# Kernel tuning notes

Measured on AMD Instinct MI355X. Metric: run time of the kernel, lower is better.

Reference implementation:

```python
import jax, jax.numpy as jnp
import numpy as np

IN_FEATURES = 512
OUT_FEATURES = 512
GRID_SIZE = 5
SPLINE_ORDER = 3
GRID_RANGE = (-3.0, 3.0)


def make_grid():
    h = (GRID_RANGE[1] - GRID_RANGE[0]) / GRID_SIZE
    g = jnp.arange(-SPLINE_ORDER, GRID_SIZE + SPLINE_ORDER + 1, dtype=jnp.float32) * h + GRID_RANGE[0]
    return jnp.broadcast_to(g, (IN_FEATURES, g.shape[0]))  # [in, grid_size+2*order+1]


def b_splines(x, grid):
    # x: [N, in] -> bases: [N, in, grid_size + spline_order]
    x = x[..., None]  # [N, in, 1]
    bases = ((x >= grid[:, :-1]) & (x < grid[:, 1:])).astype(x.dtype)
    for k in range(1, SPLINE_ORDER + 1):
        left = (x - grid[:, :-(k + 1)]) / (grid[:, k:-1] - grid[:, :-(k + 1)])
        right = (grid[:, k + 1:] - x) / (grid[:, k + 1:] - grid[:, 1:-k])
        bases = left * bases[..., :-1] + right * bases[..., 1:]
    return bases


def setup_inputs() -> dict:
    key = jax.random.key(0)
    k1, k2, k3, k4 = jax.random.split(key, 4)
    N = 32768
    bound = 1.0 / np.sqrt(IN_FEATURES)  # kaiming_uniform-ish scale
    x = jax.random.normal(k1, (N, IN_FEATURES), dtype=jnp.float32)
    base_weight = jax.random.uniform(k2, (OUT_FEATURES, IN_FEATURES), minval=-bound, maxval=bound, dtype=jnp.float32)
    spline_weight = jax.random.normal(k3, (OUT_FEATURES, IN_FEATURES, GRID_SIZE + SPLINE_ORDER), dtype=jnp.float32) * 0.1
    spline_scaler = jax.random.uniform(k4, (OUT_FEATURES, IN_FEATURES), minval=-bound, maxval=bound, dtype=jnp.float32)
    grid = make_grid()
    return {"x": x, "base_weight": base_weight, "spline_weight": spline_weight, "spline_scaler": spline_scaler, "grid": grid}


def reference(x, base_weight, spline_weight, spline_scaler, grid):
    # base branch: SiLU(x) @ W_base^T
    base_out = jnp.einsum('ni,oi->no', jax.nn.silu(x), base_weight)
    # spline branch: Cox-de Boor basis then GEMM with scaled spline weights
    b = b_splines(x, grid)  # [N, in, G+K]
    sw = spline_weight * spline_scaler[..., None]  # [out, in, G+K]
    spline_out = jnp.einsum('nik,oik->no', b, sw)
    return base_out + spline_out
```

## Files before the change

### kernel.cpp

```cpp
#include <hip/hip_runtime.h>

#define NSAMP 32768
#define INF 512
#define OUTF 512
#define NB 8
#define KSP 4096
#define KTOT 4608

typedef __attribute__((ext_vector_type(8))) short bf16x8;
typedef __attribute__((ext_vector_type(4))) float f32x4;

typedef __attribute__((address_space(1))) void gas_void;
typedef __attribute__((address_space(3))) void las_void;
#define GLL16(g, l) __builtin_amdgcn_global_load_lds( \
    (const gas_void*)(g), (las_void*)(l), 16, 0, 0)

__device__ __forceinline__ unsigned short f2bf(float f) {
  unsigned int u = __float_as_uint(f);
  u += 0x7fffu + ((u >> 16) & 1u);
  return (unsigned short)(u >> 16);
}

__device__ __forceinline__ unsigned pack_rn(float lo, float hi) {
  return __builtin_amdgcn_perm(__float_as_uint(hi) + 0x8000u,
                               __float_as_uint(lo) + 0x8000u, 0x07060302u);
}

__device__ __forceinline__ uint4 kan_basis_vec(float xv) {
  float t = __builtin_fmaf(xv, 1.0f / 1.2f, 5.5f);
  float cf = floorf(t);
  float u = t - cf;
  int j0 = (int)cf - 3;
  float omu = 1.0f - u;
  float u2 = u * u, u3 = u2 * u;
  float omu2 = omu * omu;
  float w0 = omu2 * omu;
  float w1 = __builtin_fmaf(3.f, u3, __builtin_fmaf(-6.f, u2, 4.f));
  float w2 = __builtin_fmaf(-3.f, u3,
              __builtin_fmaf(3.f, u2, __builtin_fmaf(3.f, u, 1.f)));
  float w3 = u3;
  unsigned P0 = pack_rn(w0, w1);
  unsigned P1 = pack_rn(w2, w3);
  int p = j0 & 1;
  unsigned Q0 = p ? (P0 << 16) : P0;
  unsigned Q1 = p ? __builtin_amdgcn_alignbit(P1, P0, 16) : P1;
  unsigned Q2 = p ? (P1 >> 16) : 0u;
  int D = j0 >> 1;
  uint4 r;
  r.x = (D == 0) ? Q0 : (D == -1) ? Q1 : (D == -2) ? Q2 : 0u;
  r.y = (D == 1) ? Q0 : (D ==  0) ? Q1 : (D == -1) ? Q2 : 0u;
  r.z = (D == 2) ? Q0 : (D ==  1) ? Q1 : (D ==  0) ? Q2 : 0u;
  r.w = (D == 3) ? Q0 : (D ==  2) ? Q1 : (D ==  1) ? Q2 : 0u;
  return r;
}

__global__ __launch_bounds__(256) void kan_prep_w(
    const float* __restrict__ bw, const float* __restrict__ sw,
    const float* __restrict__ sc, unsigned short* __restrict__ W) {
  int idx = blockIdx.x * 256 + threadIdx.x;
  float scv = sc[idx] * (1.0f / 6.0f);
  float4 s0 = ((const float4*)sw)[idx * 2 + 0];
  float4 s1 = ((const float4*)sw)[idx * 2 + 1];
  unsigned short v[8];
  v[0] = f2bf(s0.x * scv); v[1] = f2bf(s0.y * scv);
  v[2] = f2bf(s0.z * scv); v[3] = f2bf(s0.w * scv);
  v[4] = f2bf(s1.x * scv); v[5] = f2bf(s1.y * scv);
  v[6] = f2bf(s1.z * scv); v[7] = f2bf(s1.w * scv);
  int o = idx >> 9, i = idx & 511;
  *(bf16x8*)(W + (size_t)o * KTOT + i * NB) = *(bf16x8*)v;
  W[(size_t)o * KTOT + KSP + i] = f2bf(bw[idx]);
}

__device__ __forceinline__ void mfma_chunk(
    const unsigned short* As, const unsigned short* Bs,
    f32x4 acc[4][8], int wm, int wn, int frow, int quad) {
  const int fr7 = frow & 7;
  #pragma unroll
  for (int ks = 0; ks < 2; ++ks) {
    bf16x8 av[4], bv[8];
    const int sa = ((ks * 4 + quad) ^ fr7) * 8;
    #pragma unroll
    for (int f = 0; f < 4; ++f)
      av[f] = *(const bf16x8*)&As[(wm + f * 16 + frow) * 64 + sa];
    #pragma unroll
    for (int g = 0; g < 8; ++g)
      bv[g] = *(const bf16x8*)&Bs[(wn + g * 16 + frow) * 64 + sa];
    #pragma unroll
    for (int mf = 0; mf < 4; ++mf)
      #pragma unroll
      for (int nf = 0; nf < 8; ++nf)
        acc[mf][nf] = __builtin_amdgcn_mfma_f32_16x16x32_bf16(
            av[mf], bv[nf], acc[mf][nf], 0, 0, 0);
  }
}

__global__ __launch_bounds__(256, 2) void kan_fused(
    const float* __restrict__ x, const unsigned short* __restrict__ W,
    float* __restrict__ out) {
  __shared__ __align__(16) unsigned short As[128 * 64];
  __shared__ __align__(16) unsigned short Bs[256 * 64];
  const int tid = threadIdx.x;
  const int wave = tid >> 6;
  const int lane = tid & 63;
  const int frow = lane & 15;
  const int quad = lane >> 4;
  const int lr = lane >> 3;
  const int lc = lane & 7;
  const int mtile = blockIdx.x & 255;
  const int ntile = blockIdx.x >> 8;
  const int wm = (wave & 1) << 6;
  const int wn = (wave >> 1) << 7;

  f32x4 acc[4][8];
  #pragma unroll
  for (int i = 0; i < 4; ++i)
    #pragma unroll
    for (int j = 0; j < 8; ++j)
      acc[i][j] = (f32x4){0.f, 0.f, 0.f, 0.f};

  const unsigned short* bgp[8];
  #pragma unroll
  for (int is = 0; is < 8; ++is)
    bgp[is] = W + (size_t)(ntile * 256 + wave * 64 + is * 8 + lr) * KTOT +
              ((lc ^ lr) * 8);
  const float* xb = x + (size_t)mtile * 128 * INF;
  const float* xp[4];
  #pragma unroll
  for (int is = 0; is < 4; ++is)
    xp[is] = xb + (size_t)(wave * 32 + is * 8 + lr) * INF + lc;

  float xc[4];
  #pragma unroll
  for (int is = 0; is < 4; ++is) xc[is] = xp[is][0];

  for (int kc = 0; kc < 64; ++kc) {
    #pragma unroll
    for (int is = 0; is < 8; ++is) {
      GLL16(bgp[is], &Bs[(wave * 64 + is * 8) * 64]);
      bgp[is] += 64;
    }
    float xn[4];
    const int knext = ((kc + 1) & 63) * 8;
    #pragma unroll
    for (int is = 0; is < 4; ++is) xn[is] = xp[is][knext];

    #pragma unroll
    for (int is = 0; is < 4; ++is) {
      const int row = wave * 32 + is * 8 + lr;
      uint4 bb = kan_basis_vec(xc[is]);
      *(uint4*)&As[row * 64 + ((lc ^ lr) * 8)] = bb;
    }
    __syncthreads();
    mfma_chunk(As, Bs, acc, wm, wn, frow, quad);
    __syncthreads();
    #pragma unroll
    for (int is = 0; is < 4; ++is) xc[is] = xn[is];
  }

  for (int sc = 0; sc < 8; ++sc) {
    float4 v0[4], v1[4];
    #pragma unroll
    for (int is = 0; is < 4; ++is) {
      const int row = wave * 32 + is * 8 + lr;
      const float* xr = xb + (size_t)row * INF + sc * 64 + lc * 8;
      v0[is] = *(const float4*)xr;
      v1[is] = *(const float4*)(xr + 4);
    }
    #pragma unroll
    for (int is = 0; is < 8; ++is) {
      GLL16(bgp[is], &Bs[(wave * 64 + is * 8) * 64]);
      bgp[is] += 64;
    }
    #pragma unroll
    for (int is = 0; is < 4; ++is) {
      const int row = wave * 32 + is * 8 + lr;
      float vv[8] = {v0[is].x, v0[is].y, v0[is].z, v0[is].w,
                     v1[is].x, v1[is].y, v1[is].z, v1[is].w};
      float s[8];
      #pragma unroll
      for (int e = 0; e < 8; ++e)
        s[e] = vv[e] * __builtin_amdgcn_rcpf(1.0f + __expf(-vv[e]));
      uint4 pk;
      pk.x = pack_rn(s[0], s[1]);
      pk.y = pack_rn(s[2], s[3]);
      pk.z = pack_rn(s[4], s[5]);
      pk.w = pack_rn(s[6], s[7]);
      *(uint4*)&As[row * 64 + ((lc ^ lr) * 8)] = pk;
    }
    __syncthreads();
    mfma_chunk(As, Bs, acc, wm, wn, frow, quad);
    __syncthreads();
  }

  const size_t m0 = (size_t)mtile * 128;
  const int n0 = ntile * 256;
  #pragma unroll
  for (int mf = 0; mf < 4; ++mf)
    #pragma unroll
    for (int nf = 0; nf < 8; ++nf)
      #pragma unroll
      for (int r = 0; r < 4; ++r)
        out[(m0 + wm + mf * 16 + quad * 4 + r) * OUTF + (n0 + wn + nf * 16 + frow)] =
            acc[mf][nf][r];
}

__global__ __launch_bounds__(256) void kan_naive(
    const float* __restrict__ x, const float* __restrict__ bw,
    const float* __restrict__ sw, const float* __restrict__ sc,
    float* __restrict__ out) {
  int idx = blockIdx.x * 256 + threadIdx.x;
  int n = idx >> 9, o = idx & 511;
  const float* xr = x + (size_t)n * INF;
  float acc = 0.f;
  for (int i = 0; i < INF; ++i) {
    float xv = xr[i];
    float sil = xv / (1.0f + __expf(-xv));
    float t = (xv + 6.6f) * (1.0f / 1.2f);
    float cf = floorf(t);
    float u = t - cf;
    int j0 = (int)cf - 3;
    float omu = 1.0f - u;
    float u2 = u * u, u3 = u2 * u;
    float w[4];
    w[0] = (1.0f / 6.0f) * omu * omu * omu;
    w[1] = (1.0f / 6.0f) * (3.0f * u3 - 6.0f * u2 + 4.0f);
    w[2] = (1.0f / 6.0f) * (-3.0f * u3 + 3.0f * u2 + 3.0f * u + 1.0f);
    w[3] = (1.0f / 6.0f) * u3;
    int wi = o * INF + i;
    acc += sil * bw[wi];
    float sp = 0.f;
    #pragma unroll
    for (int m = 0; m < 4; ++m) {
      int j = j0 + m;
      if ((unsigned)j < 8u) sp += w[m] * sw[wi * NB + j];
    }
    acc += sp * sc[wi];
  }
  out[idx] = acc;
}

extern "C" void kernel_launch(void* const* d_in, const int* in_sizes, int n_in,
                              void* d_out, int out_size, void* d_ws, size_t ws_size,
                              hipStream_t stream) {
  const float* x  = (const float*)d_in[0];
  const float* bw = (const float*)d_in[1];
  const float* sw = (const float*)d_in[2];
  const float* sc = (const float*)d_in[3];
  float* out = (float*)d_out;

  const size_t wbytes = (size_t)OUTF * KTOT * 2;
  if (ws_size >= wbytes) {
    unsigned short* W = (unsigned short*)d_ws;
    kan_prep_w<<<(OUTF * INF) / 256, 256, 0, stream>>>(bw, sw, sc, W);
    kan_fused<<<(NSAMP / 128) * (OUTF / 256), 256, 0, stream>>>(x, W, out);
  } else {
    kan_naive<<<(NSAMP * OUTF) / 256, 256, 0, stream>>>(x, bw, sw, sc, out);
  }
}
```

Measured before the change: 250.1 us.

## Double-buffer spline weight tiles in LDS and overlap prefetch with MFMA

Splits the B-tile LDS buffer into two halves so the next spline-weight chunk is fetched with global_load_lds while MFMAs run on the current one. The basis tile for the following chunk is now written after the compute barrier instead of before it. A hand-placed s_waitcnt vmcnt(12) plus raw s_barrier replaces __syncthreads, and setprio raises wave priority around the MFMA blocks. This raises LDS use to about 80KB per block, and the fixed vmcnt count is fragile: on the last spline iteration it may not wait for every load of the final weight buffer.

```diff
diff --git a/kernel.cpp b/kernel.cpp
--- a/kernel.cpp
+++ b/kernel.cpp
@@ -98,7 +98,7 @@
     const float* __restrict__ x, const unsigned short* __restrict__ W,
     float* __restrict__ out) {
   __shared__ __align__(16) unsigned short As[128 * 64];
-  __shared__ __align__(16) unsigned short Bs[256 * 64];
+  __shared__ __align__(16) unsigned short Bs[2][256 * 64];
   const int tid = threadIdx.x;
   const int wave = tid >> 6;
   const int lane = tid & 63;
@@ -129,32 +129,48 @@
   for (int is = 0; is < 4; ++is)
     xp[is] = xb + (size_t)(wave * 32 + is * 8 + lr) * INF + lc;
 
-  float xc[4];
-  #pragma unroll
-  for (int is = 0; is < 4; ++is) xc[is] = xp[is][0];
+  {
+    #pragma unroll
+    for (int is = 0; is < 4; ++is) {
+      const int row = wave * 32 + is * 8 + lr;
+      uint4 bb = kan_basis_vec(xp[is][0]);
+      *(uint4*)&As[row * 64 + ((lc ^ lr) * 8)] = bb;
+    }
+    #pragma unroll
+    for (int is = 0; is < 8; ++is) {
+      GLL16(bgp[is], &Bs[0][(wave * 64 + is * 8) * 64]);
+      bgp[is] += 64;
+    }
+  }
 
   for (int kc = 0; kc < 64; ++kc) {
-    #pragma unroll
-    for (int is = 0; is < 8; ++is) {
-      GLL16(bgp[is], &Bs[(wave * 64 + is * 8) * 64]);
-      bgp[is] += 64;
+    if (kc < 63) {
+      #pragma unroll
+      for (int is = 0; is < 8; ++is) {
+        GLL16(bgp[is], &Bs[(kc + 1) & 1][(wave * 64 + is * 8) * 64]);
+        bgp[is] += 64;
+      }
     }
     float xn[4];
     const int knext = ((kc + 1) & 63) * 8;
     #pragma unroll
     for (int is = 0; is < 4; ++is) xn[is] = xp[is][knext];
 
-    #pragma unroll
-    for (int is = 0; is < 4; ++is) {
-      const int row = wave * 32 + is * 8 + lr;
-      uint4 bb = kan_basis_vec(xc[is]);
-      *(uint4*)&As[row * 64 + ((lc ^ lr) * 8)] = bb;
-    }
-    __syncthreads();
-    mfma_chunk(As, Bs, acc, wm, wn, frow, quad);
-    __syncthreads();
-    #pragma unroll
-    for (int is = 0; is < 4; ++is) xc[is] = xn[is];
+    asm volatile("s_waitcnt vmcnt(12) lgkmcnt(0)" ::: "memory");
+    asm volatile("s_barrier" ::: "memory");
+    __builtin_amdgcn_s_setprio(1);
+    mfma_chunk(As, Bs[kc & 1], acc, wm, wn, frow, quad);
+    __builtin_amdgcn_s_setprio(0);
+    asm volatile("s_barrier" ::: "memory");
+
+    if (kc < 63) {
+      #pragma unroll
+      for (int is = 0; is < 4; ++is) {
+        const int row = wave * 32 + is * 8 + lr;
+        uint4 bb = kan_basis_vec(xn[is]);
+        *(uint4*)&As[row * 64 + ((lc ^ lr) * 8)] = bb;
+      }
+    }
   }
 
   for (int sc = 0; sc < 8; ++sc) {
@@ -168,7 +184,7 @@
     }
     #pragma unroll
     for (int is = 0; is < 8; ++is) {
-      GLL16(bgp[is], &Bs[(wave * 64 + is * 8) * 64]);
+      GLL16(bgp[is], &Bs[0][(wave * 64 + is * 8) * 64]);
       bgp[is] += 64;
     }
     #pragma unroll
@@ -188,7 +204,9 @@
       *(uint4*)&As[row * 64 + ((lc ^ lr) * 8)] = pk;
     }
     __syncthreads();
-    mfma_chunk(As, Bs, acc, wm, wn, frow, quad);
+    __builtin_amdgcn_s_setprio(1);
+    mfma_chunk(As, Bs[0], acc, wm, wn, frow, quad);
+    __builtin_amdgcn_s_setprio(0);
     __syncthreads();
   }
 
```

New measurement: 253.9 us. About the same (+1.5%).

## Double-buffer weight tiles and overlap basis computation with MFMA in a unified loop

Applied to the files above, without the earlier changes.

Merges the spline and SiLU K-loops into one 72-step loop. The B tile is now double-buffered in LDS so the next chunk's global-to-LDS load is in flight while the current chunk's MFMAs run. The next A operand (basis or SiLU values) is computed in registers after the MFMA block. Hand-placed s_waitcnt counts, sched_barrier pins and s_setprio around the MFMA block control overlap, at the cost of doubling B's LDS footprint and fragile manual vmcnt bookkeeping.

```diff
diff --git a/kernel.cpp b/kernel.cpp
--- a/kernel.cpp
+++ b/kernel.cpp
@@ -14,6 +14,8 @@
 typedef __attribute__((address_space(3))) void las_void;
 #define GLL16(g, l) __builtin_amdgcn_global_load_lds( \
     (const gas_void*)(g), (las_void*)(l), 16, 0, 0)
+
+#define SCHED_PIN() __builtin_amdgcn_sched_barrier(0)
 
 __device__ __forceinline__ unsigned short f2bf(float f) {
   unsigned int u = __float_as_uint(f);
@@ -98,7 +100,7 @@
     const float* __restrict__ x, const unsigned short* __restrict__ W,
     float* __restrict__ out) {
   __shared__ __align__(16) unsigned short As[128 * 64];
-  __shared__ __align__(16) unsigned short Bs[256 * 64];
+  __shared__ __align__(16) unsigned short Bs[2][256 * 64];
   const int tid = threadIdx.x;
   const int wave = tid >> 6;
   const int lane = tid & 63;
@@ -118,78 +120,73 @@
     for (int j = 0; j < 8; ++j)
       acc[i][j] = (f32x4){0.f, 0.f, 0.f, 0.f};
 
-  const unsigned short* bgp[8];
+  const unsigned short* bg = W +
+      (size_t)(ntile * 256 + wave * 64 + lr) * KTOT + ((lc ^ lr) * 8);
+  const float* xb = x + (size_t)mtile * 128 * INF;
+  const float* xq = xb + (size_t)(wave * 32 + lr) * INF + lc;
+
+  uint4 bb[4];
   #pragma unroll
   for (int is = 0; is < 8; ++is)
-    bgp[is] = W + (size_t)(ntile * 256 + wave * 64 + is * 8 + lr) * KTOT +
-              ((lc ^ lr) * 8);
-  const float* xb = x + (size_t)mtile * 128 * INF;
-  const float* xp[4];
+    GLL16(bg + is * 36864, &Bs[0][(wave * 64 + is * 8) * 64]);
+  bg += 64;
   #pragma unroll
   for (int is = 0; is < 4; ++is)
-    xp[is] = xb + (size_t)(wave * 32 + is * 8 + lr) * INF + lc;
-
-  float xc[4];
-  #pragma unroll
-  for (int is = 0; is < 4; ++is) xc[is] = xp[is][0];
-
-  for (int kc = 0; kc < 64; ++kc) {
-    #pragma unroll
-    for (int is = 0; is < 8; ++is) {
-      GLL16(bgp[is], &Bs[(wave * 64 + is * 8) * 64]);
-      bgp[is] += 64;
-    }
+    bb[is] = kan_basis_vec(xq[is * 4096]);
+
+  for (int kc = 0; kc < 72; ++kc) {
+    #pragma unroll
+    for (int is = 0; is < 4; ++is)
+      *(uint4*)&As[(wave * 32 + is * 8 + lr) * 64 + ((lc ^ lr) * 8)] = bb[is];
     float xn[4];
-    const int knext = ((kc + 1) & 63) * 8;
-    #pragma unroll
-    for (int is = 0; is < 4; ++is) xn[is] = xp[is][knext];
-
-    #pragma unroll
-    for (int is = 0; is < 4; ++is) {
-      const int row = wave * 32 + is * 8 + lr;
-      uint4 bb = kan_basis_vec(xc[is]);
-      *(uint4*)&As[row * 64 + ((lc ^ lr) * 8)] = bb;
-    }
-    __syncthreads();
-    mfma_chunk(As, Bs, acc, wm, wn, frow, quad);
-    __syncthreads();
-    #pragma unroll
-    for (int is = 0; is < 4; ++is) xc[is] = xn[is];
-  }
-
-  for (int sc = 0; sc < 8; ++sc) {
-    float4 v0[4], v1[4];
-    #pragma unroll
-    for (int is = 0; is < 4; ++is) {
-      const int row = wave * 32 + is * 8 + lr;
-      const float* xr = xb + (size_t)row * INF + sc * 64 + lc * 8;
-      v0[is] = *(const float4*)xr;
-      v1[is] = *(const float4*)(xr + 4);
-    }
-    #pragma unroll
-    for (int is = 0; is < 8; ++is) {
-      GLL16(bgp[is], &Bs[(wave * 64 + is * 8) * 64]);
-      bgp[is] += 64;
-    }
-    #pragma unroll
-    for (int is = 0; is < 4; ++is) {
-      const int row = wave * 32 + is * 8 + lr;
-      float vv[8] = {v0[is].x, v0[is].y, v0[is].z, v0[is].w,
-                     v1[is].x, v1[is].y, v1[is].z, v1[is].w};
-      float s[8];
-      #pragma unroll
-      for (int e = 0; e < 8; ++e)
-        s[e] = vv[e] * __builtin_amdgcn_rcpf(1.0f + __expf(-vv[e]));
-      uint4 pk;
-      pk.x = pack_rn(s[0], s[1]);
-      pk.y = pack_rn(s[2], s[3]);
-      pk.z = pack_rn(s[4], s[5]);
-      pk.w = pack_rn(s[6], s[7]);
-      *(uint4*)&As[row * 64 + ((lc ^ lr) * 8)] = pk;
-    }
-    __syncthreads();
-    mfma_chunk(As, Bs, acc, wm, wn, frow, quad);
-    __syncthreads();
+    if (kc < 63) {
+      #pragma unroll
+      for (int is = 0; is < 4; ++is) xn[is] = xq[is * 4096 + (kc + 1) * 8];
+    }
+    if (kc < 71) {
+      #pragma unroll
+      for (int is = 0; is < 8; ++is)
+        GLL16(bg + is * 36864, &Bs[(kc + 1) & 1][(wave * 64 + is * 8) * 64]);
+      bg += 64;
+    }
+    SCHED_PIN();
+    if (kc < 63)      asm volatile("s_waitcnt vmcnt(12) lgkmcnt(0)");
+    else if (kc < 71) asm volatile("s_waitcnt vmcnt(8) lgkmcnt(0)");
+    else              asm volatile("s_waitcnt vmcnt(0) lgkmcnt(0)");
+    __builtin_amdgcn_s_barrier();
+    SCHED_PIN();
+
+    __builtin_amdgcn_s_setprio(1);
+    mfma_chunk(As, Bs[kc & 1], acc, wm, wn, frow, quad);
+    __builtin_amdgcn_s_setprio(0);
+    if (kc < 63) {
+      #pragma unroll
+      for (int is = 0; is < 4; ++is) bb[is] = kan_basis_vec(xn[is]);
+    } else if (kc < 71) {
+      const int sc = kc + 1 - 64;
+      #pragma unroll
+      for (int is = 0; is < 4; ++is) {
+        const float* xr =
+            xb + (size_t)(wave * 32 + is * 8 + lr) * INF + sc * 64 + lc * 8;
+        float4 a0 = *(const float4*)xr;
+        float4 a1 = *(const float4*)(xr + 4);
+        float vv[8] = {a0.x, a0.y, a0.z, a0.w, a1.x, a1.y, a1.z, a1.w};
+        float s[8];
+        #pragma unroll
+        for (int e = 0; e < 8; ++e)
+          s[e] = vv[e] * __builtin_amdgcn_rcpf(1.0f + __expf(-vv[e]));
+        uint4 pk;
+        pk.x = pack_rn(s[0], s[1]);
+        pk.y = pack_rn(s[2], s[3]);
+        pk.z = pack_rn(s[4], s[5]);
+        pk.w = pack_rn(s[6], s[7]);
+        bb[is] = pk;
+      }
+    }
+    SCHED_PIN();
+    asm volatile("s_waitcnt lgkmcnt(0)");
+    __builtin_amdgcn_s_barrier();
+    SCHED_PIN();
   }
 
   const size_t m0 = (size_t)mtile * 128;
```

After: 261.6 us. 1.05x slower.

## Double-buffer weight tiles and compute spline basis directly in MFMA registers

Applied to the files above, without the earlier changes.

The weight tile in LDS is now double-buffered, so the next chunk's global-to-LDS load is issued before the current chunk's MFMAs, and one barrier per iteration is removed. In the spline phase the basis vectors are computed straight into the A-operand registers from x values each lane loads itself, which bypasses the As shared-memory round trip. In exchange each lane recomputes its basis values and LDS use grows. The wait on the async loads relies on the barrier ordering, which makes the correctness of the buffer swap subtle.

```diff
diff --git a/kernel.cpp b/kernel.cpp
--- a/kernel.cpp
+++ b/kernel.cpp
@@ -94,11 +94,34 @@
   }
 }
 
+__device__ __forceinline__ void mfma_chunk_regA(
+    const float xn[8], const unsigned short* Bs,
+    f32x4 acc[4][8], int wn, int frow, int quad) {
+  const int fr7 = frow & 7;
+  #pragma unroll
+  for (int ks = 0; ks < 2; ++ks) {
+    bf16x8 bv[8];
+    const int sa = ((ks * 4 + quad) ^ fr7) * 8;
+    #pragma unroll
+    for (int g = 0; g < 8; ++g)
+      bv[g] = *(const bf16x8*)&Bs[(wn + g * 16 + frow) * 64 + sa];
+    #pragma unroll
+    for (int mf = 0; mf < 4; ++mf) {
+      uint4 ab = kan_basis_vec(xn[mf * 2 + ks]);
+      bf16x8 av = __builtin_bit_cast(bf16x8, ab);
+      #pragma unroll
+      for (int nf = 0; nf < 8; ++nf)
+        acc[mf][nf] = __builtin_amdgcn_mfma_f32_16x16x32_bf16(
+            av, bv[nf], acc[mf][nf], 0, 0, 0);
+    }
+  }
+}
+
 __global__ __launch_bounds__(256, 2) void kan_fused(
     const float* __restrict__ x, const unsigned short* __restrict__ W,
     float* __restrict__ out) {
   __shared__ __align__(16) unsigned short As[128 * 64];
-  __shared__ __align__(16) unsigned short Bs[256 * 64];
+  __shared__ __align__(16) unsigned short Bs[2][256 * 64];
   const int tid = threadIdx.x;
   const int wave = tid >> 6;
   const int lane = tid & 63;
@@ -118,46 +141,44 @@
     for (int j = 0; j < 8; ++j)
       acc[i][j] = (f32x4){0.f, 0.f, 0.f, 0.f};
 
-  const unsigned short* bgp[8];
-  #pragma unroll
-  for (int is = 0; is < 8; ++is)
-    bgp[is] = W + (size_t)(ntile * 256 + wave * 64 + is * 8 + lr) * KTOT +
-              ((lc ^ lr) * 8);
+  const unsigned short* bg = W +
+      (size_t)(ntile * 256 + wave * 64 + lr) * KTOT + ((lc ^ lr) * 8);
   const float* xb = x + (size_t)mtile * 128 * INF;
   const float* xp[4];
   #pragma unroll
-  for (int is = 0; is < 4; ++is)
-    xp[is] = xb + (size_t)(wave * 32 + is * 8 + lr) * INF + lc;
-
-  float xc[4];
-  #pragma unroll
-  for (int is = 0; is < 4; ++is) xc[is] = xp[is][0];
+  for (int mf = 0; mf < 4; ++mf)
+    xp[mf] = xb + (size_t)(wm + mf * 16 + frow) * INF + quad;
+
+  #pragma unroll
+  for (int is = 0; is < 8; ++is)
+    GLL16(bg + is * 36864, &Bs[0][(wave * 64 + is * 8) * 64]);
+  bg += 64;
+  float xn[8];
+  #pragma unroll
+  for (int mf = 0; mf < 4; ++mf)
+    #pragma unroll
+    for (int ks = 0; ks < 2; ++ks)
+      xn[mf * 2 + ks] = xp[mf][ks * 4];
 
   for (int kc = 0; kc < 64; ++kc) {
-    #pragma unroll
-    for (int is = 0; is < 8; ++is) {
-      GLL16(bgp[is], &Bs[(wave * 64 + is * 8) * 64]);
-      bgp[is] += 64;
-    }
-    float xn[4];
-    const int knext = ((kc + 1) & 63) * 8;
-    #pragma unroll
-    for (int is = 0; is < 4; ++is) xn[is] = xp[is][knext];
-
-    #pragma unroll
-    for (int is = 0; is < 4; ++is) {
-      const int row = wave * 32 + is * 8 + lr;
-      uint4 bb = kan_basis_vec(xc[is]);
-      *(uint4*)&As[row * 64 + ((lc ^ lr) * 8)] = bb;
-    }
     __syncthreads();
-    mfma_chunk(As, Bs, acc, wm, wn, frow, quad);
+    #pragma unroll
+    for (int is = 0; is < 8; ++is)
+      GLL16(bg + is * 36864, &Bs[(kc + 1) & 1][(wave * 64 + is * 8) * 64]);
+    bg += 64;
+    mfma_chunk_regA(xn, Bs[kc & 1], acc, wn, frow, quad);
+    if (kc < 63) {
+      const int kn = (kc + 1) * 8;
+      #pragma unroll
+      for (int mf = 0; mf < 4; ++mf)
+        #pragma unroll
+        for (int ks = 0; ks < 2; ++ks)
+          xn[mf * 2 + ks] = xp[mf][kn + ks * 4];
+    }
+  }
+
+  for (int sc = 0; sc < 8; ++sc) {
     __syncthreads();
-    #pragma unroll
-    for (int is = 0; is < 4; ++is) xc[is] = xn[is];
-  }
-
-  for (int sc = 0; sc < 8; ++sc) {
     float4 v0[4], v1[4];
     #pragma unroll
     for (int is = 0; is < 4; ++is) {
@@ -166,10 +187,11 @@
       v0[is] = *(const float4*)xr;
       v1[is] = *(const float4*)(xr + 4);
     }
-    #pragma unroll
-    for (int is = 0; is < 8; ++is) {
-      GLL16(bgp[is], &Bs[(wave * 64 + is * 8) * 64]);
-      bgp[is] += 64;
+    if (sc < 7) {
+      #pragma unroll
+      for (int is = 0; is < 8; ++is)
+        GLL16(bg + is * 36864, &Bs[(sc + 1) & 1][(wave * 64 + is * 8) * 64]);
+      bg += 64;
     }
     #pragma unroll
     for (int is = 0; is < 4; ++is) {
@@ -188,8 +210,7 @@
       *(uint4*)&As[row * 64 + ((lc ^ lr) * 8)] = pk;
     }
     __syncthreads();
-    mfma_chunk(As, Bs, acc, wm, wn, frow, quad);
-    __syncthreads();
+    mfma_chunk(As, Bs[sc & 1], acc, wm, wn, frow, quad);
   }
 
   const size_t m0 = (size_t)mtile * 128;
```

Measured after the change: 371.4 us. +48.5%, slower.
